# Kernel tuning notes

Measured on AMD Instinct MI355X. Metric: run time of the kernel, lower is better.

## Reference

```python
import jax, jax.numpy as jnp
import numpy as np

B, H, L, TAU, THETA = 8192, 256, 4, 8, 8


def setup_inputs() -> dict:
    key = jax.random.key(0)
    ks = jax.random.split(key, 16)
    w = lambda k, shape: (jax.random.normal(k, shape, jnp.float32) * 0.02)
    return {
        "x": jax.random.normal(ks[0], (B, H), jnp.float32),
        "t_att": jax.random.normal(ks[1], (L, TAU, B, H), jnp.float32),
        "s_att": jax.random.normal(ks[2], (L, TAU, B, H), jnp.float32),
        "embed_w": w(ks[3], (H, H)),
        "embed_b": jnp.zeros((H,), jnp.float32),
        "wtn": w(ks[4], (L, H, H)),
        "btn": jnp.zeros((L, H), jnp.float32),
        "wsn": w(ks[5], (L, H, H)),
        "bsn": jnp.zeros((L, H), jnp.float32),
        "wt": w(ks[6], (L, 3 * H, H)),
        "bt": jnp.zeros((L, 3 * H), jnp.float32),
        "ws": w(ks[7], (L, 3 * H, H)),
        "bs": jnp.zeros((L, 3 * H), jnp.float32),
        "out_w": w(ks[8], (H, H)),
        "out_b": jnp.zeros((H,), jnp.float32),
    }


def _forward(x, t_att, s_att, embed_w, embed_b, wtn, btn, wsn, bsn, wt, bt, ws, bs, out_w, out_b):
    n_layers, tau = t_att.shape[0], t_att.shape[1]
    b, h = x.shape
    scale = 1.0 / np.sqrt(h).astype(np.float32)
    theta = THETA

    S = x @ embed_w.T + embed_b  # embed: [B, H]
    # rolling spatial buffers, start as theta zero entries
    t_sp = jnp.zeros((theta, b, h), x.dtype)
    s_sp = jnp.zeros((theta, b, h), x.dtype)

    for i in range(n_layers):
        T_last = t_att[i, -1]  # [B, H]
        # append current S_t / last T_t to spatial buffers, keep last theta
        s_sp = jnp.concatenate([s_sp[1:], S[None]], axis=0)
        t_sp = jnp.concatenate([t_sp[1:], T_last[None]], axis=0)
        # s_att[i].append(S_t); slice last tau -> keys include current S
        s_keys = jnp.concatenate([s_att[i, 1:], S[None]], axis=0)  # [tau, B, H]
        t_vals = t_att[i]  # [tau, B, H]

        s_next = S @ wsn[i].T + bsn[i]
        t_next = T_last @ wtn[i].T + btn[i]

        # temporal attention over last-tau history
        w_t = jax.nn.softmax(jnp.einsum('kbh,bh->kb', s_keys, s_next) * scale, axis=0)
        T_trend = jnp.einsum('kb,kbh->bh', w_t, t_vals)
        t_gate = jax.nn.sigmoid(t_next)
        T_fusion = T_last * t_gate + (1.0 - t_gate) * T_trend

        # spatial attention over last-theta buffer
        w_s = jax.nn.softmax(jnp.einsum('kbh,bh->kb', t_sp, t_next) * scale, axis=0)
        S_trend = jnp.einsum('kb,kbh->bh', w_s, s_sp)
        s_gate = jax.nn.sigmoid(s_next)
        S_fusion = S * s_gate + (1.0 - s_gate) * S_trend

        Tc = T_fusion @ wt[i].T + bt[i]  # [B, 3H]
        Sc = S_fusion @ ws[i].T + bs[i]
        t_g, t_t_, t_s_ = jnp.split(Tc, 3, axis=-1)
        s_g, s_t_, s_s_ = jnp.split(Sc, 3, axis=-1)
        Tg = jax.nn.sigmoid(t_g)
        Sg = jax.nn.sigmoid(s_g)
        # T_new feeds the (stateful) history; S carries to next layer
        S = Sg * s_s_ + (1.0 - Sg) * t_s_

    return jnp.tanh(S @ out_w.T + out_b)


def reference(x, t_att, s_att, embed_w, embed_b, wtn, btn, wsn, bsn, wt, bt, ws, bs, out_w, out_b):
    return _forward(x, t_att, s_att, embed_w, embed_b, wtn, btn, wsn, bsn, wt, bt, ws, bs, out_w, out_b)
```

## Files before the change

kernel.cpp:

```cpp
#include <hip/hip_runtime.h>
#include <cmath>

typedef __attribute__((ext_vector_type(8))) short short8;
typedef __attribute__((ext_vector_type(4))) float f32x4;
typedef __attribute__((ext_vector_type(4))) unsigned short us4;
typedef unsigned short u16;

#define BATCH 8192
#define HDIM  256
static constexpr size_t BH = (size_t)BATCH * HDIM;

__device__ __forceinline__ u16 f2bf(float f) {
    union { float f; unsigned u; } v; v.f = f;
    unsigned r = v.u + 0x7FFFu + ((v.u >> 16) & 1u);
    return (u16)(r >> 16);
}
__device__ __forceinline__ float bf2f(u16 u) {
    union { unsigned u; float f; } v; v.u = ((unsigned)u) << 16;
    return v.f;
}
__device__ __forceinline__ float wred(float v) {
#pragma unroll
    for (int o = 32; o > 0; o >>= 1) v += __shfl_xor(v, o);
    return v;
}
__device__ __forceinline__ float sigmoidf_(float x) {
    return 1.f / (1.f + __expf(-x));
}
__device__ __forceinline__ short8 cvt8(const float* p) {
    f32x4 lo = *(const f32x4*)p, hi = *(const f32x4*)(p + 4);
    short8 t;
    t[0] = (short)f2bf(lo[0]); t[1] = (short)f2bf(lo[1]);
    t[2] = (short)f2bf(lo[2]); t[3] = (short)f2bf(lo[3]);
    t[4] = (short)f2bf(hi[0]); t[5] = (short)f2bf(hi[1]);
    t[6] = (short)f2bf(hi[2]); t[7] = (short)f2bf(hi[3]);
    return t;
}

__global__ __launch_bounds__(256) void convert_weights(
    const float* __restrict__ embed_w, const float* __restrict__ wtn,
    const float* __restrict__ wsn, const float* __restrict__ wt,
    const float* __restrict__ ws, const float* __restrict__ out_w,
    u16* __restrict__ dst)
{
    int idx = blockIdx.x * 256 + threadIdx.x;
    int e = idx * 4;
    if (e >= 22 * 65536) return;
    int c = e >> 16, o = e & 65535;
    const float* src;
    if (c == 0)      src = embed_w + o;
    else if (c < 5)  src = wtn + (size_t)(c - 1) * 65536 + o;
    else if (c < 9)  src = wsn + (size_t)(c - 5) * 65536 + o;
    else if (c < 13) src = wt + (size_t)(c - 9) * 768 * 256 + 512 * 256 + o;
    else if (c < 17) src = ws + (size_t)(c - 13) * 768 * 256 + o;
    else if (c < 21) src = ws + (size_t)(c - 17) * 768 * 256 + 512 * 256 + o;
    else             src = out_w + o;
    f32x4 v = *(const f32x4*)src;
    us4 r;
#pragma unroll
    for (int j = 0; j < 4; ++j) r[j] = f2bf(v[j]);
    *(us4*)(dst + e) = r;
}

#define PAD 264
__global__ __launch_bounds__(512, 4) void stau_mega(
    const float* __restrict__ x,
    const float* __restrict__ t_att, const float* __restrict__ s_att,
    const u16* __restrict__ Wbf,
    const float* __restrict__ embed_b,
    const float* __restrict__ btn, const float* __restrict__ bsn,
    const float* __restrict__ bt, const float* __restrict__ bs,
    const float* __restrict__ out_b,
    float* __restrict__ outp)
{
    __shared__ __align__(16) u16 S_lds[5][16][PAD];
    __shared__ __align__(16) u16 sn_lds[16][PAD];
    __shared__ __align__(16) u16 tn_lds[16][PAD];
    __shared__ __align__(16) u16 tf_lds[16][PAD];
    __shared__ __align__(16) u16 sf_lds[16][PAD];

    const int lane = threadIdx.x & 63;
    const int wave = threadIdx.x >> 6;
    const int lr = lane & 15;
    const int kg = lane >> 4;
    const int row0 = blockIdx.x * 16;
    const float scale = 0.0625f;

    {
        const int n0 = wave * 32;
        f32x4 acc[2] = {};
        for (int k0 = 0; k0 < 256; k0 += 32) {
            int k = k0 + kg * 8;
            short8 a = cvt8(x + (size_t)(row0 + lr) * 256 + k);
#pragma unroll
            for (int nf = 0; nf < 2; ++nf) {
                short8 b = *(const short8*)(Wbf + (size_t)(n0 + nf * 16 + lr) * 256 + k);
                acc[nf] = __builtin_amdgcn_mfma_f32_16x16x32_bf16(a, b, acc[nf], 0, 0, 0);
            }
        }
#pragma unroll
        for (int nf = 0; nf < 2; ++nf) {
            int n = n0 + nf * 16 + lr;
            float bn = embed_b[n];
#pragma unroll
            for (int r = 0; r < 4; ++r)
                S_lds[0][kg * 4 + r][n] = f2bf(acc[nf][r] + bn);
        }
    }
    __syncthreads();

    for (int i = 0; i < 4; ++i) {
        {
            const int g = wave >> 2;
            const int n0 = (wave & 3) * 64;
            const u16* Wm = Wbf + (size_t)((g ? 1 : 5) + i) * 65536;
            const float* bias = (g ? btn : bsn) + i * 256;
            f32x4 acc[4] = {};
            for (int k0 = 0; k0 < 256; k0 += 32) {
                int k = k0 + kg * 8;
                short8 a;
                if (g == 0) a = *(const short8*)(&S_lds[i][lr][k]);
                else        a = cvt8(t_att + ((size_t)i * 8 + 7) * BH + (size_t)(row0 + lr) * 256 + k);
#pragma unroll
                for (int nf = 0; nf < 4; ++nf) {
                    short8 b = *(const short8*)(Wm + (size_t)(n0 + nf * 16 + lr) * 256 + k);
                    acc[nf] = __builtin_amdgcn_mfma_f32_16x16x32_bf16(a, b, acc[nf], 0, 0, 0);
                }
            }
            u16 (*dst)[PAD] = g ? tn_lds : sn_lds;
#pragma unroll
            for (int nf = 0; nf < 4; ++nf) {
                int n = n0 + nf * 16 + lr;
                float bn = bias[n];
#pragma unroll
                for (int r = 0; r < 4; ++r)
                    dst[kg * 4 + r][n] = f2bf(acc[nf][r] + bn);
            }
        }
        __syncthreads();

        for (int rr = wave * 2; rr < wave * 2 + 2; ++rr) {
            const size_t ro = (size_t)(row0 + rr) * 256 + lane * 4;
            us4 snu = *(const us4*)&sn_lds[rr][lane * 4];
            us4 tnu = *(const us4*)&tn_lds[rr][lane * 4];
            us4 scu = *(const us4*)&S_lds[i][rr][lane * 4];
            float sn[4], tn[4], Sc[4];
#pragma unroll
            for (int j = 0; j < 4; ++j) { sn[j] = bf2f(snu[j]); tn[j] = bf2f(tnu[j]); Sc[j] = bf2f(scu[j]); }

            const float* sa = s_att + (size_t)i * 8 * BH + ro;
            const float* ta = t_att + (size_t)i * 8 * BH + ro;

            float lt[8];
#pragma unroll
            for (int kk = 0; kk < 7; ++kk) {
                f32x4 v = *(const f32x4*)(sa + (size_t)(kk + 1) * BH);
                lt[kk] = wred(v[0] * sn[0] + v[1] * sn[1] + v[2] * sn[2] + v[3] * sn[3]) * scale;
            }
            lt[7] = wred(Sc[0] * sn[0] + Sc[1] * sn[1] + Sc[2] * sn[2] + Sc[3] * sn[3]) * scale;

            float m = lt[0];
#pragma unroll
            for (int kk = 1; kk < 8; ++kk) m = fmaxf(m, lt[kk]);
            float w8[8], den = 0.f;
#pragma unroll
            for (int kk = 0; kk < 8; ++kk) { w8[kk] = __expf(lt[kk] - m); den += w8[kk]; }
            float inv = 1.f / den;

            float Tt[4] = {0.f, 0.f, 0.f, 0.f}, Tl[4];
#pragma unroll
            for (int kk = 0; kk < 8; ++kk) {
                f32x4 v = *(const f32x4*)(ta + (size_t)kk * BH);
#pragma unroll
                for (int j = 0; j < 4; ++j) Tt[j] += w8[kk] * v[j];
                if (kk == 7) { Tl[0] = v[0]; Tl[1] = v[1]; Tl[2] = v[2]; Tl[3] = v[3]; }
            }
            us4 ot;
#pragma unroll
            for (int j = 0; j < 4; ++j) {
                float g = sigmoidf_(tn[j]);
                ot[j] = f2bf(Tl[j] * g + (1.f - g) * Tt[j] * inv);
            }
            *(us4*)&tf_lds[rr][lane * 4] = ot;

            float msx = 0.f;
            float dens = (float)(7 - i);
            float St[4] = {0.f, 0.f, 0.f, 0.f};
            for (int jj = 0; jj <= i; ++jj) {
                f32x4 v = *(const f32x4*)(t_att + ((size_t)jj * 8 + 7) * BH + ro);
                float p = wred(v[0] * tn[0] + v[1] * tn[1] + v[2] * tn[2] + v[3] * tn[3]) * scale;
                us4 shu = *(const us4*)&S_lds[jj][rr][lane * 4];
                if (p > msx) {
                    float c = __expf(msx - p);
                    dens *= c; St[0] *= c; St[1] *= c; St[2] *= c; St[3] *= c;
                    msx = p;
                }
                float w = __expf(p - msx);
                dens += w;
#pragma unroll
                for (int j = 0; j < 4; ++j) St[j] += w * bf2f(shu[j]);
            }
            float invs = 1.f / dens;
            us4 os;
#pragma unroll
            for (int j = 0; j < 4; ++j) {
                float g = sigmoidf_(sn[j]);
                os[j] = f2bf(Sc[j] * g + (1.f - g) * St[j] * invs);
            }
            *(us4*)&sf_lds[rr][lane * 4] = os;
        }
        __syncthreads();

        {
            const int n0 = wave * 32;
            const u16* Wt3 = Wbf + (size_t)(9  + i) * 65536;
            const u16* Ws1 = Wbf + (size_t)(13 + i) * 65536;
            const u16* Ws3 = Wbf + (size_t)(17 + i) * 65536;
            f32x4 aT[2] = {}, aG[2] = {}, aS[2] = {};
            for (int k0 = 0; k0 < 256; k0 += 32) {
                int k = k0 + kg * 8;
                short8 at = *(const short8*)(&tf_lds[lr][k]);
                short8 as = *(const short8*)(&sf_lds[lr][k]);
#pragma unroll
                for (int nf = 0; nf < 2; ++nf) {
                    size_t wo = (size_t)(n0 + nf * 16 + lr) * 256 + k;
                    aT[nf] = __builtin_amdgcn_mfma_f32_16x16x32_bf16(at, *(const short8*)(Wt3 + wo), aT[nf], 0, 0, 0);
                    aG[nf] = __builtin_amdgcn_mfma_f32_16x16x32_bf16(as, *(const short8*)(Ws1 + wo), aG[nf], 0, 0, 0);
                    aS[nf] = __builtin_amdgcn_mfma_f32_16x16x32_bf16(as, *(const short8*)(Ws3 + wo), aS[nf], 0, 0, 0);
                }
            }
            const float* b1 = bt + i * 768 + 512;
            const float* b2 = bs + i * 768;
            const float* b3 = bs + i * 768 + 512;
#pragma unroll
            for (int nf = 0; nf < 2; ++nf) {
                int n = n0 + nf * 16 + lr;
                float bb1 = b1[n], bb2 = b2[n], bb3 = b3[n];
#pragma unroll
                for (int r = 0; r < 4; ++r) {
                    float gv = sigmoidf_(aG[nf][r] + bb2);
                    float v = gv * (aS[nf][r] + bb3) + (1.f - gv) * (aT[nf][r] + bb1);
                    S_lds[i + 1][kg * 4 + r][n] = f2bf(v);
                }
            }
        }
        __syncthreads();
    }

    {
        const int n0 = wave * 32;
        const u16* Wo = Wbf + (size_t)21 * 65536;
        f32x4 acc[2] = {};
        for (int k0 = 0; k0 < 256; k0 += 32) {
            int k = k0 + kg * 8;
            short8 a = *(const short8*)(&S_lds[4][lr][k]);
#pragma unroll
            for (int nf = 0; nf < 2; ++nf) {
                short8 b = *(const short8*)(Wo + (size_t)(n0 + nf * 16 + lr) * 256 + k);
                acc[nf] = __builtin_amdgcn_mfma_f32_16x16x32_bf16(a, b, acc[nf], 0, 0, 0);
            }
        }
#pragma unroll
        for (int nf = 0; nf < 2; ++nf) {
            int n = n0 + nf * 16 + lr;
            float bn = out_b[n];
#pragma unroll
            for (int r = 0; r < 4; ++r)
                outp[(size_t)(row0 + kg * 4 + r) * 256 + n] = tanhf(acc[nf][r] + bn);
        }
    }
}

extern "C" void kernel_launch(void* const* d_in, const int* in_sizes, int n_in,
                              void* d_out, int out_size, void* d_ws, size_t ws_size,
                              hipStream_t stream)
{
    (void)in_sizes; (void)n_in; (void)out_size; (void)ws_size;
    const float* x       = (const float*)d_in[0];
    const float* t_att   = (const float*)d_in[1];
    const float* s_att   = (const float*)d_in[2];
    const float* embed_w = (const float*)d_in[3];
    const float* embed_b = (const float*)d_in[4];
    const float* wtn     = (const float*)d_in[5];
    const float* btn     = (const float*)d_in[6];
    const float* wsn     = (const float*)d_in[7];
    const float* bsn     = (const float*)d_in[8];
    const float* wt      = (const float*)d_in[9];
    const float* bt      = (const float*)d_in[10];
    const float* ws_in   = (const float*)d_in[11];
    const float* bs      = (const float*)d_in[12];
    const float* out_w   = (const float*)d_in[13];
    const float* out_b   = (const float*)d_in[14];

    u16* Wbf = (u16*)d_ws;

    convert_weights<<<1408, 256, 0, stream>>>(embed_w, wtn, wsn, wt, ws_in, out_w, Wbf);

    stau_mega<<<BATCH / 16, 512, 0, stream>>>(
        x, t_att, s_att, Wbf, embed_b, btn, bsn, bt, bs, out_b, (float*)d_out);
}
```

Before: 284.4 us.

## Use 16 waves per block and batch attention-history loads ahead of reductions

```diff
diff --git a/kernel.cpp b/kernel.cpp
--- a/kernel.cpp
+++ b/kernel.cpp
@@ -63,7 +63,7 @@
 }
 
 #define PAD 264
-__global__ __launch_bounds__(512, 4) void stau_mega(
+__global__ __launch_bounds__(1024, 8) void stau_mega(
     const float* __restrict__ x,
     const float* __restrict__ t_att, const float* __restrict__ s_att,
     const u16* __restrict__ Wbf,
@@ -84,62 +84,49 @@
     const int lr = lane & 15;
     const int kg = lane >> 4;
     const int row0 = blockIdx.x * 16;
+    const int n0 = wave * 16;
     const float scale = 0.0625f;
 
     {
-        const int n0 = wave * 32;
-        f32x4 acc[2] = {};
+        f32x4 acc = {};
         for (int k0 = 0; k0 < 256; k0 += 32) {
             int k = k0 + kg * 8;
             short8 a = cvt8(x + (size_t)(row0 + lr) * 256 + k);
-#pragma unroll
-            for (int nf = 0; nf < 2; ++nf) {
-                short8 b = *(const short8*)(Wbf + (size_t)(n0 + nf * 16 + lr) * 256 + k);
-                acc[nf] = __builtin_amdgcn_mfma_f32_16x16x32_bf16(a, b, acc[nf], 0, 0, 0);
-            }
-        }
-#pragma unroll
-        for (int nf = 0; nf < 2; ++nf) {
-            int n = n0 + nf * 16 + lr;
-            float bn = embed_b[n];
-#pragma unroll
-            for (int r = 0; r < 4; ++r)
-                S_lds[0][kg * 4 + r][n] = f2bf(acc[nf][r] + bn);
-        }
+            short8 b = *(const short8*)(Wbf + (size_t)(n0 + lr) * 256 + k);
+            acc = __builtin_amdgcn_mfma_f32_16x16x32_bf16(a, b, acc, 0, 0, 0);
+        }
+        float bn = embed_b[n0 + lr];
+#pragma unroll
+        for (int r = 0; r < 4; ++r)
+            S_lds[0][kg * 4 + r][n0 + lr] = f2bf(acc[r] + bn);
     }
     __syncthreads();
 
     for (int i = 0; i < 4; ++i) {
         {
-            const int g = wave >> 2;
-            const int n0 = (wave & 3) * 64;
-            const u16* Wm = Wbf + (size_t)((g ? 1 : 5) + i) * 65536;
-            const float* bias = (g ? btn : bsn) + i * 256;
-            f32x4 acc[4] = {};
+            const u16* Wsn = Wbf + (size_t)(5 + i) * 65536;
+            const u16* Wtn = Wbf + (size_t)(1 + i) * 65536;
+            f32x4 accS = {}, accT = {};
             for (int k0 = 0; k0 < 256; k0 += 32) {
                 int k = k0 + kg * 8;
-                short8 a;
-                if (g == 0) a = *(const short8*)(&S_lds[i][lr][k]);
-                else        a = cvt8(t_att + ((size_t)i * 8 + 7) * BH + (size_t)(row0 + lr) * 256 + k);
-#pragma unroll
-                for (int nf = 0; nf < 4; ++nf) {
-                    short8 b = *(const short8*)(Wm + (size_t)(n0 + nf * 16 + lr) * 256 + k);
-                    acc[nf] = __builtin_amdgcn_mfma_f32_16x16x32_bf16(a, b, acc[nf], 0, 0, 0);
-                }
-            }
-            u16 (*dst)[PAD] = g ? tn_lds : sn_lds;
-#pragma unroll
-            for (int nf = 0; nf < 4; ++nf) {
-                int n = n0 + nf * 16 + lr;
-                float bn = bias[n];
-#pragma unroll
-                for (int r = 0; r < 4; ++r)
-                    dst[kg * 4 + r][n] = f2bf(acc[nf][r] + bn);
+                short8 aS = *(const short8*)(&S_lds[i][lr][k]);
+                short8 aT = cvt8(t_att + ((size_t)i * 8 + 7) * BH + (size_t)(row0 + lr) * 256 + k);
+                size_t wo = (size_t)(n0 + lr) * 256 + k;
+                accS = __builtin_amdgcn_mfma_f32_16x16x32_bf16(aS, *(const short8*)(Wsn + wo), accS, 0, 0, 0);
+                accT = __builtin_amdgcn_mfma_f32_16x16x32_bf16(aT, *(const short8*)(Wtn + wo), accT, 0, 0, 0);
+            }
+            float bS = bsn[i * 256 + n0 + lr];
+            float bT = btn[i * 256 + n0 + lr];
+#pragma unroll
+            for (int r = 0; r < 4; ++r) {
+                sn_lds[kg * 4 + r][n0 + lr] = f2bf(accS[r] + bS);
+                tn_lds[kg * 4 + r][n0 + lr] = f2bf(accT[r] + bT);
             }
         }
         __syncthreads();
 
-        for (int rr = wave * 2; rr < wave * 2 + 2; ++rr) {
+        {
+            const int rr = wave;
             const size_t ro = (size_t)(row0 + rr) * 256 + lane * 4;
             us4 snu = *(const us4*)&sn_lds[rr][lane * 4];
             us4 tnu = *(const us4*)&tn_lds[rr][lane * 4];
@@ -151,12 +138,19 @@
             const float* sa = s_att + (size_t)i * 8 * BH + ro;
             const float* ta = t_att + (size_t)i * 8 * BH + ro;
 
+            f32x4 sav[7], tav[8], tsp[4];
+#pragma unroll
+            for (int kk = 0; kk < 7; ++kk) sav[kk] = *(const f32x4*)(sa + (size_t)(kk + 1) * BH);
+#pragma unroll
+            for (int kk = 0; kk < 8; ++kk) tav[kk] = *(const f32x4*)(ta + (size_t)kk * BH);
+#pragma unroll
+            for (int jj = 0; jj < 4; ++jj)
+                if (jj <= i) tsp[jj] = *(const f32x4*)(t_att + ((size_t)jj * 8 + 7) * BH + ro);
+
             float lt[8];
 #pragma unroll
-            for (int kk = 0; kk < 7; ++kk) {
-                f32x4 v = *(const f32x4*)(sa + (size_t)(kk + 1) * BH);
-                lt[kk] = wred(v[0] * sn[0] + v[1] * sn[1] + v[2] * sn[2] + v[3] * sn[3]) * scale;
-            }
+            for (int kk = 0; kk < 7; ++kk)
+                lt[kk] = wred(sav[kk][0] * sn[0] + sav[kk][1] * sn[1] + sav[kk][2] * sn[2] + sav[kk][3] * sn[3]) * scale;
             lt[7] = wred(Sc[0] * sn[0] + Sc[1] * sn[1] + Sc[2] * sn[2] + Sc[3] * sn[3]) * scale;
 
             float m = lt[0];
@@ -167,39 +161,39 @@
             for (int kk = 0; kk < 8; ++kk) { w8[kk] = __expf(lt[kk] - m); den += w8[kk]; }
             float inv = 1.f / den;
 
-            float Tt[4] = {0.f, 0.f, 0.f, 0.f}, Tl[4];
-#pragma unroll
-            for (int kk = 0; kk < 8; ++kk) {
-                f32x4 v = *(const f32x4*)(ta + (size_t)kk * BH);
-#pragma unroll
-                for (int j = 0; j < 4; ++j) Tt[j] += w8[kk] * v[j];
-                if (kk == 7) { Tl[0] = v[0]; Tl[1] = v[1]; Tl[2] = v[2]; Tl[3] = v[3]; }
-            }
+            float Tt[4] = {0.f, 0.f, 0.f, 0.f};
+#pragma unroll
+            for (int kk = 0; kk < 8; ++kk)
+#pragma unroll
+                for (int j = 0; j < 4; ++j) Tt[j] += w8[kk] * tav[kk][j];
             us4 ot;
 #pragma unroll
             for (int j = 0; j < 4; ++j) {
                 float g = sigmoidf_(tn[j]);
-                ot[j] = f2bf(Tl[j] * g + (1.f - g) * Tt[j] * inv);
+                ot[j] = f2bf(tav[7][j] * g + (1.f - g) * Tt[j] * inv);
             }
             *(us4*)&tf_lds[rr][lane * 4] = ot;
 
-            float msx = 0.f;
-            float dens = (float)(7 - i);
+            float lsp[4];
+#pragma unroll
+            for (int jj = 0; jj < 4; ++jj)
+                if (jj <= i)
+                    lsp[jj] = wred(tsp[jj][0] * tn[0] + tsp[jj][1] * tn[1] + tsp[jj][2] * tn[2] + tsp[jj][3] * tn[3]) * scale;
+            float ms = 0.f;
+#pragma unroll
+            for (int jj = 0; jj < 4; ++jj)
+                if (jj <= i) ms = fmaxf(ms, lsp[jj]);
+            float dens = (float)(7 - i) * __expf(-ms);
             float St[4] = {0.f, 0.f, 0.f, 0.f};
-            for (int jj = 0; jj <= i; ++jj) {
-                f32x4 v = *(const f32x4*)(t_att + ((size_t)jj * 8 + 7) * BH + ro);
-                float p = wred(v[0] * tn[0] + v[1] * tn[1] + v[2] * tn[2] + v[3] * tn[3]) * scale;
-                us4 shu = *(const us4*)&S_lds[jj][rr][lane * 4];
-                if (p > msx) {
-                    float c = __expf(msx - p);
-                    dens *= c; St[0] *= c; St[1] *= c; St[2] *= c; St[3] *= c;
-                    msx = p;
+#pragma unroll
+            for (int jj = 0; jj < 4; ++jj)
+                if (jj <= i) {
+                    float w = __expf(lsp[jj] - ms);
+                    dens += w;
+                    us4 shu = *(const us4*)&S_lds[jj][rr][lane * 4];
+#pragma unroll
+                    for (int j = 0; j < 4; ++j) St[j] += w * bf2f(shu[j]);
                 }
-                float w = __expf(p - msx);
-                dens += w;
-#pragma unroll
-                for (int j = 0; j < 4; ++j) St[j] += w * bf2f(shu[j]);
-            }
             float invs = 1.f / dens;
             us4 os;
 #pragma unroll
@@ -212,62 +206,45 @@
         __syncthreads();
 
         {
-            const int n0 = wave * 32;
             const u16* Wt3 = Wbf + (size_t)(9  + i) * 65536;
             const u16* Ws1 = Wbf + (size_t)(13 + i) * 65536;
             const u16* Ws3 = Wbf + (size_t)(17 + i) * 65536;
-            f32x4 aT[2] = {}, aG[2] = {}, aS[2] = {};
+            f32x4 aT = {}, aG = {}, aS = {};
             for (int k0 = 0; k0 < 256; k0 += 32) {
                 int k = k0 + kg * 8;
                 short8 at = *(const short8*)(&tf_lds[lr][k]);
                 short8 as = *(const short8*)(&sf_lds[lr][k]);
-#pragma unroll
-                for (int nf = 0; nf < 2; ++nf) {
-                    size_t wo = (size_t)(n0 + nf * 16 + lr) * 256 + k;
-                    aT[nf] = __builtin_amdgcn_mfma_f32_16x16x32_bf16(at, *(const short8*)(Wt3 + wo), aT[nf], 0, 0, 0);
-                    aG[nf] = __builtin_amdgcn_mfma_f32_16x16x32_bf16(as, *(const short8*)(Ws1 + wo), aG[nf], 0, 0, 0);
-                    aS[nf] = __builtin_amdgcn_mfma_f32_16x16x32_bf16(as, *(const short8*)(Ws3 + wo), aS[nf], 0, 0, 0);
-                }
-            }
-            const float* b1 = bt + i * 768 + 512;
-            const float* b2 = bs + i * 768;
-            const float* b3 = bs + i * 768 + 512;
-#pragma unroll
-            for (int nf = 0; nf < 2; ++nf) {
-                int n = n0 + nf * 16 + lr;
-                float bb1 = b1[n], bb2 = b2[n], bb3 = b3[n];
-#pragma unroll
-                for (int r = 0; r < 4; ++r) {
-                    float gv = sigmoidf_(aG[nf][r] + bb2);
-                    float v = gv * (aS[nf][r] + bb3) + (1.f - gv) * (aT[nf][r] + bb1);
-                    S_lds[i + 1][kg * 4 + r][n] = f2bf(v);
-                }
+                size_t wo = (size_t)(n0 + lr) * 256 + k;
+                aT = __builtin_amdgcn_mfma_f32_16x16x32_bf16(at, *(const short8*)(Wt3 + wo), aT, 0, 0, 0);
+                aG = __builtin_amdgcn_mfma_f32_16x16x32_bf16(as, *(const short8*)(Ws1 + wo), aG, 0, 0, 0);
+                aS = __builtin_amdgcn_mfma_f32_16x16x32_bf16(as, *(const short8*)(Ws3 + wo), aS, 0, 0, 0);
+            }
+            float bb1 = bt[i * 768 + 512 + n0 + lr];
+            float bb2 = bs[i * 768 + n0 + lr];
+            float bb3 = bs[i * 768 + 512 + n0 + lr];
+#pragma unroll
+            for (int r = 0; r < 4; ++r) {
+                float gv = sigmoidf_(aG[r] + bb2);
+                float v = gv * (aS[r] + bb3) + (1.f - gv) * (aT[r] + bb1);
+                S_lds[i + 1][kg * 4 + r][n0 + lr] = f2bf(v);
             }
         }
         __syncthreads();
     }
 
     {
-        const int n0 = wave * 32;
         const u16* Wo = Wbf + (size_t)21 * 65536;
-        f32x4 acc[2] = {};
+        f32x4 acc = {};
         for (int k0 = 0; k0 < 256; k0 += 32) {
             int k = k0 + kg * 8;
             short8 a = *(const short8*)(&S_lds[4][lr][k]);
-#pragma unroll
-            for (int nf = 0; nf < 2; ++nf) {
-                short8 b = *(const short8*)(Wo + (size_t)(n0 + nf * 16 + lr) * 256 + k);
-                acc[nf] = __builtin_amdgcn_mfma_f32_16x16x32_bf16(a, b, acc[nf], 0, 0, 0);
-            }
-        }
-#pragma unroll
-        for (int nf = 0; nf < 2; ++nf) {
-            int n = n0 + nf * 16 + lr;
-            float bn = out_b[n];
-#pragma unroll
-            for (int r = 0; r < 4; ++r)
-                outp[(size_t)(row0 + kg * 4 + r) * 256 + n] = tanhf(acc[nf][r] + bn);
-        }
+            short8 b = *(const short8*)(Wo + (size_t)(n0 + lr) * 256 + k);
+            acc = __builtin_amdgcn_mfma_f32_16x16x32_bf16(a, b, acc, 0, 0, 0);
+        }
+        float bn = out_b[n0 + lr];
+#pragma unroll
+        for (int r = 0; r < 4; ++r)
+            outp[(size_t)(row0 + kg * 4 + r) * 256 + n0 + lr] = tanhf(acc[r] + bn);
     }
 }
 
@@ -296,6 +273,6 @@
 
     convert_weights<<<1408, 256, 0, stream>>>(embed_w, wtn, wsn, wt, ws_in, out_w, Wbf);
 
-    stau_mega<<<BATCH / 16, 512, 0, stream>>>(
+    stau_mega<<<BATCH / 16, 1024, 0, stream>>>(
         x, t_att, s_att, Wbf, embed_b, btn, bsn, bt, bs, out_b, (float*)d_out);
 }
```

Result: slower. 412.5 us (+45.0%).
